# Kernel tuning notes

Hardware: AMD Instinct MI355X
Metric: run time of the kernel (lower is better)

## Reference

```python
import math
import jax, jax.numpy as jnp
import numpy as np

B, S, D, H = 4, 1024, 768, 12  # batch, seq, hidden, heads (ViT-Base)
HD = D // H                     # head size = 64
EPS = 1e-12                     # F.normalize eps


def setup_inputs() -> dict:
    key = jax.random.key(0)
    ks = jax.random.split(key, 7)
    s = 0.02
    return {
        "hidden_states": jax.random.normal(ks[0], (B, S, D), dtype=jnp.float32),
        "Wq": jax.random.normal(ks[1], (D, D), dtype=jnp.float32) * s,
        "bq": jax.random.normal(ks[2], (D,), dtype=jnp.float32) * s,
        "Wv": jax.random.normal(ks[3], (D, D), dtype=jnp.float32) * s,
        "bv": jax.random.normal(ks[4], (D,), dtype=jnp.float32) * s,
        "Wo": jax.random.normal(ks[5], (D, D), dtype=jnp.float32) * s,
        "bo": jax.random.normal(ks[6], (D,), dtype=jnp.float32) * s,
    }


def _split_heads(x):
    # [B,S,D] -> [B,H,S,hd]
    b, s, _ = x.shape
    return x.reshape(b, s, H, HD).transpose(0, 2, 1, 3)


def reference(hidden_states, Wq, bq, Wv, bv, Wo, bo):
    b, s, d_model = hidden_states.shape
    # Linear layers (torch Linear: x @ W^T + b; here W stored already transposed)
    mixed_q = hidden_states @ Wq + bq          # key == query in this module
    mixed_v = hidden_states @ Wv + bv
    q = _split_heads(mixed_q)                  # [B,H,S,hd]
    v = _split_heads(mixed_v)                  # [B,H,S,hd]

    # symmetric self-attention (Q @ Q^T)
    scores = jnp.einsum("bhsd,bhtd->bhst", q, q) / math.sqrt(HD)
    probs1 = jax.nn.softmax(scores, axis=-1)                 # [B,H,S,S]
    probs = 0.5 * (probs1 + probs1.transpose(0, 1, 3, 2))    # symmetrize

    # F.normalize(value_layer, dim=2): L2-normalize along the SEQUENCE axis
    vnorm = jnp.maximum(jnp.sqrt(jnp.sum(v * v, axis=2, keepdims=True)), EPS)
    V = v / vnorm                                            # [B,H,S,hd]

    # random-walk Laplacian: D^{-1}(D - P) = I - P / rowsum  (diag structure exploited,
    # same math as diag_embed + matmul in the original)
    dvec = probs.sum(axis=3)                                 # [B,H,S]
    Pn = probs / dvec[..., :, None]                          # D^{-1} P
    LrwV = V - jnp.einsum("bhst,bhtd->bhsd", Pn, V)          # L_rw @ V

    # trace( sum_{b,h} V^T L_rw V ) = sum over all (b,h,s,d) of V * (L_rw V)
    denom = jnp.float32(HD * H * b)
    tr = jnp.abs(jnp.sum(V * LrwV)) / denom

    # orthogonality regularizer: sum (V^T V - I)^2
    VtV = jnp.einsum("bhsd,bhse->bhde", V, V)                # [B,H,hd,hd]
    regular_term = jnp.sum((VtV - jnp.eye(HD, dtype=V.dtype)) ** 2) / denom

    # context = P @ V  (is_last=False)
    ctx = jnp.einsum("bhst,bhtd->bhsd", probs, v)
    ctx = ctx.transpose(0, 2, 1, 3).reshape(b, s, d_model)
    attention_output = ctx @ Wo + bo                         # dropout = identity (p=0)
    return (attention_output, tr, regular_term, mixed_q, mixed_q)
```

## Files before the change

### kernel.cpp

```cpp
#include <hip/hip_runtime.h>
#include <math.h>

constexpr float SCALE = 0.125f;

typedef __attribute__((ext_vector_type(8))) short bf8;
typedef __attribute__((ext_vector_type(8))) unsigned short u16x8;
typedef __attribute__((ext_vector_type(4))) float f32x4;

static __device__ __forceinline__ unsigned short f2bf(float f) {
    unsigned int u = __float_as_uint(f);
    u += 0x7fffu + ((u >> 16) & 1u);
    return (unsigned short)(u >> 16);
}
static __device__ __forceinline__ float bf2f(unsigned short h) {
    return __uint_as_float(((unsigned int)h) << 16);
}
static __device__ __forceinline__ bf8 ld8(const unsigned short* p) {
    return *reinterpret_cast<const bf8*>(p);
}
static __device__ __forceinline__ unsigned int cvtpk(float lo, float hi) {
    unsigned int r;
    asm("v_cvt_pk_bf16_f32 %0, %1, %2" : "=v"(r) : "v"(lo), "v"(hi));
    return r;
}

__global__ __launch_bounds__(256)
void k_prep(const float* __restrict__ Wq, const float* __restrict__ Wv,
            unsigned short* __restrict__ WTq, unsigned short* __restrict__ WTv)
{
    __shared__ unsigned short T[64 * 72];
    const int bid = blockIdx.x;
    const bool isQ = (bid < 144);
    const int lb = isQ ? bid : bid - 144;
    const float* __restrict__ W = isQ ? Wq : Wv;
    unsigned short* __restrict__ WT = isQ ? WTq : WTv;
    const int n0 = (lb % 12) * 64;
    const int k0 = (lb / 12) * 64;
    const int tid = threadIdx.x;
    const int r  = tid >> 2;
    const int c0 = (tid & 3) * 16;
    const float* src = &W[(size_t)(k0 + r) * 768 + n0 + c0];
    #pragma unroll
    for (int q = 0; q < 4; ++q) {
        const float4 v = *reinterpret_cast<const float4*>(src + q * 4);
        uint2 pk;
        pk.x = cvtpk(v.x, v.y);
        pk.y = cvtpk(v.z, v.w);
        *reinterpret_cast<uint2*>(&T[r * 72 + c0 + q * 4]) = pk;
    }
    __syncthreads();
    const int n  = tid >> 2;
    const int kc = (tid & 3) * 16;
    u16x8 o0, o1;
    #pragma unroll
    for (int i = 0; i < 8; ++i) o0[i] = T[(kc + i) * 72 + n];
    #pragma unroll
    for (int i = 0; i < 8; ++i) o1[i] = T[(kc + 8 + i) * 72 + n];
    unsigned short* dst = WT + (size_t)(n0 + n) * 768 + k0 + kc;
    *reinterpret_cast<u16x8*>(dst)     = o0;
    *reinterpret_cast<u16x8*>(dst + 8) = o1;
}

__global__ __launch_bounds__(256)
void k_wt(const float* __restrict__ W, unsigned short* __restrict__ WT)
{
    __shared__ unsigned short T[64 * 72];
    const int n0 = blockIdx.x * 64;
    const int k0 = blockIdx.y * 64;
    const int tid = threadIdx.x;
    const int r  = tid >> 2;
    const int c0 = (tid & 3) * 16;
    const float* src = &W[(size_t)(k0 + r) * 768 + n0 + c0];
    #pragma unroll
    for (int q = 0; q < 4; ++q) {
        const float4 v = *reinterpret_cast<const float4*>(src + q * 4);
        uint2 pk;
        pk.x = cvtpk(v.x, v.y);
        pk.y = cvtpk(v.z, v.w);
        *reinterpret_cast<uint2*>(&T[r * 72 + c0 + q * 4]) = pk;
    }
    __syncthreads();
    const int n  = tid >> 2;
    const int kc = (tid & 3) * 16;
    u16x8 o0, o1;
    #pragma unroll
    for (int i = 0; i < 8; ++i) o0[i] = T[(kc + i) * 72 + n];
    #pragma unroll
    for (int i = 0; i < 8; ++i) o1[i] = T[(kc + 8 + i) * 72 + n];
    unsigned short* dst = WT + (size_t)(n0 + n) * 768 + k0 + kc;
    *reinterpret_cast<u16x8*>(dst)     = o0;
    *reinterpret_cast<u16x8*>(dst + 8) = o1;
}

__global__ __launch_bounds__(256)
void k_gemm_qv(const float* __restrict__ X,
               const unsigned short* __restrict__ WTq,
               const unsigned short* __restrict__ WTv,
               const float* __restrict__ bq, const float* __restrict__ bv,
               float* __restrict__ mq1, float* __restrict__ mq2,
               unsigned short* __restrict__ qb, unsigned short* __restrict__ mvb)
{
    __shared__ unsigned short As[64 * 72];
    __shared__ unsigned short Bs[128 * 72];
    const int m0 = blockIdx.x * 64;
    const bool isQ = (blockIdx.y < 6);
    const int n0 = (isQ ? blockIdx.y : blockIdx.y - 6) * 128;
    const unsigned short* __restrict__ WT = isQ ? WTq : WTv;
    const float* __restrict__ bias = isQ ? bq : bv;
    const int tid = threadIdx.x;
    const int wave = tid >> 6, lane = tid & 63, lm = lane & 15, lg = lane >> 4;
    const int wn = wave;

    f32x4 acc[4][2];
    #pragma unroll
    for (int mi = 0; mi < 4; ++mi)
        #pragma unroll
        for (int ni = 0; ni < 2; ++ni) acc[mi][ni] = (f32x4){0.f, 0.f, 0.f, 0.f};

    for (int k0 = 0; k0 < 768; k0 += 64) {
        #pragma unroll
        for (int it = 0; it < 4; ++it) {
            const int idx = tid + it * 256;
            const int arow = idx >> 4;
            const int ac4  = (idx & 15) * 4;
            const float4 v = *reinterpret_cast<const float4*>(
                &X[(size_t)(m0 + arow) * 768 + k0 + ac4]);
            uint2 pk;
            pk.x = cvtpk(v.x, v.y);
            pk.y = cvtpk(v.z, v.w);
            *reinterpret_cast<uint2*>(&As[arow * 72 + ac4]) = pk;
            const int brow = idx >> 3;
            const int bc8  = (idx & 7) * 8;
            *reinterpret_cast<u16x8*>(&Bs[brow * 72 + bc8]) =
                *reinterpret_cast<const u16x8*>(&WT[(size_t)(n0 + brow) * 768 + k0 + bc8]);
        }
        __syncthreads();
        #pragma unroll
        for (int ks = 0; ks < 2; ++ks) {
            bf8 af[4], bfr[2];
            #pragma unroll
            for (int mi = 0; mi < 4; ++mi)
                af[mi] = *reinterpret_cast<const bf8*>(
                    &As[(mi * 16 + lm) * 72 + ks * 32 + lg * 8]);
            #pragma unroll
            for (int ni = 0; ni < 2; ++ni)
                bfr[ni] = *reinterpret_cast<const bf8*>(
                    &Bs[(wn * 32 + ni * 16 + lm) * 72 + ks * 32 + lg * 8]);
            #pragma unroll
            for (int mi = 0; mi < 4; ++mi)
                #pragma unroll
                for (int ni = 0; ni < 2; ++ni)
                    acc[mi][ni] = __builtin_amdgcn_mfma_f32_16x16x32_bf16(
                        af[mi], bfr[ni], acc[mi][ni], 0, 0, 0);
        }
        __syncthreads();
    }
    #pragma unroll
    for (int ni = 0; ni < 2; ++ni) {
        const int c = n0 + wn * 32 + ni * 16 + lm;
        const float bcol = bias[c];
        #pragma unroll
        for (int mi = 0; mi < 4; ++mi)
            #pragma unroll
            for (int j = 0; j < 4; ++j) {
                const int r = m0 + mi * 16 + lg * 4 + j;
                const float v = acc[mi][ni][j] + bcol;
                const size_t off = (size_t)r * 768 + c;
                if (isQ) {
                    mq1[off] = v;
                    mq2[off] = v;
                    qb[off]  = f2bf(v);
                } else {
                    mvb[off] = f2bf(v);
                }
            }
    }
}

__global__ __launch_bounds__(256)
void k_gemm_one(const unsigned short* __restrict__ Xb,
                const unsigned short* __restrict__ WT,
                const float* __restrict__ bias, float* __restrict__ out)
{
    __shared__ unsigned short As[64 * 72];
    __shared__ unsigned short Bs[64 * 72];
    const int m0 = blockIdx.x * 64;
    const int n0 = blockIdx.y * 64;
    const int tid = threadIdx.x;
    const int w = tid >> 6, lane = tid & 63, lm = lane & 15, lg = lane >> 4;

    f32x4 acc[4];
    #pragma unroll
    for (int ni = 0; ni < 4; ++ni) acc[ni] = (f32x4){0.f, 0.f, 0.f, 0.f};

    for (int k0 = 0; k0 < 768; k0 += 64) {
        #pragma unroll
        for (int it = 0; it < 2; ++it) {
            const int idx = tid + it * 256;
            const int row = idx >> 3;
            const int c8  = (idx & 7) * 8;
            *reinterpret_cast<u16x8*>(&As[row * 72 + c8]) =
                *reinterpret_cast<const u16x8*>(&Xb[(size_t)(m0 + row) * 768 + k0 + c8]);
            *reinterpret_cast<u16x8*>(&Bs[row * 72 + c8]) =
                *reinterpret_cast<const u16x8*>(&WT[(size_t)(n0 + row) * 768 + k0 + c8]);
        }
        __syncthreads();
        #pragma unroll
        for (int ks = 0; ks < 2; ++ks) {
            const bf8 af = *reinterpret_cast<const bf8*>(
                &As[(w * 16 + lm) * 72 + ks * 32 + lg * 8]);
            #pragma unroll
            for (int ni = 0; ni < 4; ++ni) {
                const bf8 bfr = *reinterpret_cast<const bf8*>(
                    &Bs[(ni * 16 + lm) * 72 + ks * 32 + lg * 8]);
                acc[ni] = __builtin_amdgcn_mfma_f32_16x16x32_bf16(af, bfr, acc[ni], 0, 0, 0);
            }
        }
        __syncthreads();
    }
    #pragma unroll
    for (int ni = 0; ni < 4; ++ni) {
        const int c = n0 + ni * 16 + lm;
        const float bcol = bias[c];
        #pragma unroll
        for (int j = 0; j < 4; ++j) {
            const int r = m0 + w * 16 + lg * 4 + j;
            out[(size_t)r * 768 + c] = acc[ni][j] + bcol;
        }
    }
}

__global__ __launch_bounds__(256)
void k_pass1T(const unsigned short* __restrict__ qb,
              const unsigned short* __restrict__ mvb,
              unsigned short* __restrict__ vT,
              float* __restrict__ a, float* __restrict__ nrmp)
{
    __shared__ __align__(16) unsigned short Kb[2][64 * 72];
    const int bid = blockIdx.x;
    const int st = (bid >> 3) & 15;
    const int bh = (bid & 7) + 8 * (bid >> 7);
    const int b = bh / 12, h = bh % 12;
    const int s0 = st * 64;
    const int tid = threadIdx.x;
    const int w = tid >> 6, lane = tid & 63, lm = lane & 15, lg = lane >> 4;
    const size_t qoff = (size_t)(b * 1024) * 768 + h * 64;

    {
        const int r  = tid >> 2;
        const int c0 = (tid & 3) * 16;
        const unsigned short* src = mvb + (size_t)(b * 1024 + s0 + r) * 768 + h * 64 + c0;
        const u16x8 x0 = *reinterpret_cast<const u16x8*>(src);
        const u16x8 x1 = *reinterpret_cast<const u16x8*>(src + 8);
        *reinterpret_cast<u16x8*>(&Kb[0][r * 72 + c0])     = x0;
        *reinterpret_cast<u16x8*>(&Kb[0][r * 72 + c0 + 8]) = x1;
        __syncthreads();
        const int dd  = tid >> 2;
        const int sc0 = (tid & 3) * 16;
        u16x8 o0, o1;
        float ps = 0.f;
        #pragma unroll
        for (int k = 0; k < 8; ++k) {
            o0[k] = Kb[0][(sc0 + k) * 72 + dd];
            const float v = bf2f(o0[k]);
            ps = fmaf(v, v, ps);
        }
        #pragma unroll
        for (int k = 0; k < 8; ++k) {
            o1[k] = Kb[0][(sc0 + 8 + k) * 72 + dd];
            const float v = bf2f(o1[k]);
            ps = fmaf(v, v, ps);
        }
        ps += __shfl_xor(ps, 1);
        ps += __shfl_xor(ps, 2);
        if ((tid & 3) == 0) nrmp[(size_t)(bh * 16 + st) * 64 + dd] = ps;
        unsigned short* dst = vT + (size_t)bh * 65536 + (size_t)dd * 1024 + s0 + sc0;
        *reinterpret_cast<u16x8*>(dst)     = o0;
        *reinterpret_cast<u16x8*>(dst + 8) = o1;
        __syncthreads();
    }

    const unsigned short* srow_p = qb + qoff + (size_t)(s0 + 16 * w + lm) * 768;
    const bf8 qs0 = ld8(srow_p + 8 * lg);
    const bf8 qs1 = ld8(srow_p + 32 + 8 * lg);
    const f32x4 z = {0.f, 0.f, 0.f, 0.f};
    float r = 0.f;
    const int sr = tid >> 2;
    const int sc = (tid & 3) << 4;

    u16x8 kr0 = *reinterpret_cast<const u16x8*>(qb + qoff + (size_t)sr * 768 + sc);
    u16x8 kr1 = *reinterpret_cast<const u16x8*>(qb + qoff + (size_t)sr * 768 + sc + 8);
    *reinterpret_cast<u16x8*>(&Kb[0][sr * 72 + sc])     = kr0;
    *reinterpret_cast<u16x8*>(&Kb[0][sr * 72 + sc + 8]) = kr1;
    __syncthreads();
    int cur = 0;

    for (int tt = 0; tt < 16; ++tt) {
        if (tt < 15) {
            const size_t rg = qoff + (size_t)((tt + 1) * 64 + sr) * 768 + sc;
            kr0 = *reinterpret_cast<const u16x8*>(qb + rg);
            kr1 = *reinterpret_cast<const u16x8*>(qb + rg + 8);
        }
        #pragma unroll
        for (int nf = 0; nf < 4; ++nf) {
            const bf8 ka0 = *reinterpret_cast<const bf8*>(
                &Kb[cur][(16 * nf + lm) * 72 + 8 * lg]);
            const bf8 ka1 = *reinterpret_cast<const bf8*>(
                &Kb[cur][(16 * nf + lm) * 72 + 32 + 8 * lg]);
            f32x4 ef = __builtin_amdgcn_mfma_f32_16x16x32_bf16(ka0, qs0, z, 0, 0, 0);
            ef = __builtin_amdgcn_mfma_f32_16x16x32_bf16(ka1, qs1, ef, 0, 0, 0);
            r += __expf(ef[0] * SCALE) + __expf(ef[1] * SCALE)
               + __expf(ef[2] * SCALE) + __expf(ef[3] * SCALE);
        }
        if (tt < 15) {
            *reinterpret_cast<u16x8*>(&Kb[cur ^ 1][sr * 72 + sc])     = kr0;
            *reinterpret_cast<u16x8*>(&Kb[cur ^ 1][sr * 72 + sc + 8]) = kr1;
        }
        __syncthreads();
        cur ^= 1;
    }
    r += __shfl_xor(r, 16);
    r += __shfl_xor(r, 32);
    if (lg == 0) a[(size_t)bh * 1024 + s0 + 16 * w + lm] = 1.f / r;
}

__global__ __launch_bounds__(256)
void k_normfin(const float* __restrict__ nrmp, float* __restrict__ inv_n,
               float* __restrict__ t1p)
{
    const int bh = blockIdx.x;
    const int tid = threadIdx.x;
    __shared__ float t1s[64];
    if (tid < 64) {
        float s = 0.f;
        for (int st = 0; st < 16; ++st)
            s += nrmp[(size_t)(bh * 16 + st) * 64 + tid];
        const float n = fmaxf(sqrtf(s), 1e-12f);
        const float iv = 1.f / n;
        inv_n[bh * 64 + tid] = iv;
        t1s[tid] = s * iv * iv;
    }
    __syncthreads();
    if (tid == 0) {
        float t = 0.f;
        for (int k = 0; k < 64; ++k) t += t1s[k];
        t1p[bh] = t;
    }
}

__global__ __launch_bounds__(256)
void k_pass2(const unsigned short* __restrict__ qb,
             const unsigned short* __restrict__ vT,
             const unsigned short* __restrict__ mvb,
             const float* __restrict__ a,
             const float* __restrict__ invn,
             unsigned short* __restrict__ ctxb,
             float* __restrict__ t2p)
{
    __shared__ __align__(16) unsigned short Kb[2][64 * 72];
    __shared__ __align__(16) unsigned short Vb[2][64 * 72];
    __shared__ __align__(16) unsigned short F_lds[4 * 16 * 72];
    __shared__ float red[256];
    const int bid = blockIdx.x;
    const int st = (bid >> 3) & 15;
    const int bh = (bid & 7) + 8 * (bid >> 7);
    const int b = bh / 12, h = bh % 12;
    const int s0 = st * 64;
    const int tid = threadIdx.x;
    const int w = tid >> 6, lane = tid & 63, lm = lane & 15, lg = lane >> 4;
    const size_t qoff = (size_t)(b * 1024) * 768 + h * 64;
    const unsigned short* srow_p = qb + qoff + (size_t)(s0 + 16 * w + lm) * 768;
    const bf8 qs0 = ld8(srow_p + 8 * lg);
    const bf8 qs1 = ld8(srow_p + 32 + 8 * lg);
    const unsigned short* vbase = vT + (size_t)bh * 65536;
    const float* abase = a + (size_t)bh * 1024;
    const float a_s = abase[s0 + 16 * w + lm];
    unsigned short* Frow = &F_lds[w * 1152 + lm * 72];
    float inv2[4];
    #pragma unroll
    for (int nf = 0; nf < 4; ++nf) {
        const float iv = invn[bh * 64 + lm + 16 * nf];
        inv2[nf] = iv * iv;
    }
    const f32x4 z = {0.f, 0.f, 0.f, 0.f};
    f32x4 acc[4];
    #pragma unroll
    for (int nf = 0; nf < 4; ++nf) acc[nf] = z;
    float sF = 0.f;
    const int sr = tid >> 2;
    const int sc = (tid & 3) << 4;

    u16x8 kr0 = *reinterpret_cast<const u16x8*>(qb + qoff + (size_t)sr * 768 + sc);
    u16x8 kr1 = *reinterpret_cast<const u16x8*>(qb + qoff + (size_t)sr * 768 + sc + 8);
    u16x8 vr0 = *reinterpret_cast<const u16x8*>(vbase + (size_t)sr * 1024 + sc);
    u16x8 vr1 = *reinterpret_cast<const u16x8*>(vbase + (size_t)sr * 1024 + sc + 8);
    *reinterpret_cast<u16x8*>(&Kb[0][sr * 72 + sc])     = kr0;
    *reinterpret_cast<u16x8*>(&Kb[0][sr * 72 + sc + 8]) = kr1;
    *reinterpret_cast<u16x8*>(&Vb[0][sr * 72 + sc])     = vr0;
    *reinterpret_cast<u16x8*>(&Vb[0][sr * 72 + sc + 8]) = vr1;
    __syncthreads();
    int cur = 0;

    for (int tt = 0; tt < 16; ++tt) {
        const int t0 = tt * 64;
        if (tt < 15) {
            const size_t kg = qoff + (size_t)(t0 + 64 + sr) * 768 + sc;
            kr0 = *reinterpret_cast<const u16x8*>(qb + kg);
            kr1 = *reinterpret_cast<const u16x8*>(qb + kg + 8);
            const size_t vg = (size_t)sr * 1024 + t0 + 64 + sc;
            vr0 = *reinterpret_cast<const u16x8*>(vbase + vg);
            vr1 = *reinterpret_cast<const u16x8*>(vbase + vg + 8);
        }
        f32x4 ef[4];
        #pragma unroll
        for (int nf = 0; nf < 4; ++nf) {
            const bf8 ka0 = *reinterpret_cast<const bf8*>(
                &Kb[cur][(16 * nf + lm) * 72 + 8 * lg]);
            const bf8 ka1 = *reinterpret_cast<const bf8*>(
                &Kb[cur][(16 * nf + lm) * 72 + 32 + 8 * lg]);
            ef[nf] = __builtin_amdgcn_mfma_f32_16x16x32_bf16(ka0, qs0, z, 0, 0, 0);
            ef[nf] = __builtin_amdgcn_mfma_f32_16x16x32_bf16(ka1, qs1, ef[nf], 0, 0, 0);
        }
        #pragma unroll
        for (int nf = 0; nf < 4; ++nf) {
            const float4 af = *reinterpret_cast<const float4*>(
                abase + t0 + 16 * nf + 4 * lg);
            const float f0 = __expf(ef[nf][0] * SCALE) * (a_s + af.x);
            const float f1 = __expf(ef[nf][1] * SCALE) * (a_s + af.y);
            const float f2 = __expf(ef[nf][2] * SCALE) * (a_s + af.z);
            const float f3 = __expf(ef[nf][3] * SCALE) * (a_s + af.w);
            sF += (f0 + f1) + (f2 + f3);
            uint2 pk;
            pk.x = cvtpk(f0, f1);
            pk.y = cvtpk(f2, f3);
            *reinterpret_cast<uint2*>(&Frow[16 * nf + 4 * lg]) = pk;
        }
        #pragma unroll
        for (int ks = 0; ks < 2; ++ks) {
            const bf8 fa = *reinterpret_cast<const bf8*>(&Frow[32 * ks + 8 * lg]);
            #pragma unroll
            for (int nf = 0; nf < 4; ++nf) {
                const bf8 vfr = *reinterpret_cast<const bf8*>(
                    &Vb[cur][(16 * nf + lm) * 72 + 32 * ks + 8 * lg]);
                acc[nf] = __builtin_amdgcn_mfma_f32_16x16x32_bf16(fa, vfr, acc[nf], 0, 0, 0);
            }
        }
        if (tt < 15) {
            *reinterpret_cast<u16x8*>(&Kb[cur ^ 1][sr * 72 + sc])     = kr0;
            *reinterpret_cast<u16x8*>(&Kb[cur ^ 1][sr * 72 + sc + 8]) = kr1;
            *reinterpret_cast<u16x8*>(&Vb[cur ^ 1][sr * 72 + sc])     = vr0;
            *reinterpret_cast<u16x8*>(&Vb[cur ^ 1][sr * 72 + sc + 8]) = vr1;
        }
        __syncthreads();
        cur ^= 1;
    }
    sF += __shfl_xor(sF, 16);
    sF += __shfl_xor(sF, 32);

    float t2 = 0.f;
    #pragma unroll
    for (int j = 0; j < 4; ++j) {
        const int srow = s0 + 16 * w + 4 * lg + j;
        const float sFj = __shfl(sF, 4 * lg + j);
        const float rdv = 2.f / sFj;
        const size_t rowoff = (size_t)(b * 1024 + srow) * 768 + h * 64;
        #pragma unroll
        for (int nf = 0; nf < 4; ++nf) {
            const int d = lm + 16 * nf;
            const float cf = 0.5f * acc[nf][j];
            ctxb[rowoff + d] = f2bf(cf);
            const float vv = bf2f(mvb[rowoff + d]);
            t2 = fmaf(vv * cf, inv2[nf] * rdv, t2);
        }
    }
    red[tid] = t2;
    __syncthreads();
    for (int k = 128; k >= 1; k >>= 1) {
        if (tid < k) red[tid] += red[tid + k];
        __syncthreads();
    }
    if (tid == 0) t2p[bh * 16 + st] = red[0];
}

__global__ __launch_bounds__(256)
void k_reg(const unsigned short* __restrict__ vT, const float* __restrict__ invn,
           float* __restrict__ regp)
{
    const int bh = blockIdx.x;
    const int tid = threadIdx.x;
    const int w = tid >> 6, lane = tid & 63, lm = lane & 15, lg = lane >> 4;
    const unsigned short* base = vT + (size_t)bh * 65536;
    const unsigned short* arowp = base + (size_t)(16 * w + lm) * 1024;
    const f32x4 z = {0.f, 0.f, 0.f, 0.f};
    f32x4 acc[4];
    #pragma unroll
    for (int nf = 0; nf < 4; ++nf) acc[nf] = z;
    for (int kb = 0; kb < 32; ++kb) {
        const int t0 = kb * 32 + 8 * lg;
        const bf8 av = ld8(arowp + t0);
        #pragma unroll
        for (int nf = 0; nf < 4; ++nf) {
            const bf8 bv = ld8(base + (size_t)(lm + 16 * nf) * 1024 + t0);
            acc[nf] = __builtin_amdgcn_mfma_f32_16x16x32_bf16(av, bv, acc[nf], 0, 0, 0);
        }
    }
    float part = 0.f;
    #pragma unroll
    for (int nf = 0; nf < 4; ++nf) {
        const int d2 = lm + 16 * nf;
        const float i2 = invn[bh * 64 + d2];
        #pragma unroll
        for (int j = 0; j < 4; ++j) {
            const int d1 = 16 * w + 4 * lg + j;
            const float g = acc[nf][j] * invn[bh * 64 + d1] * i2;
            const float diff = g - ((d1 == d2) ? 1.f : 0.f);
            part = fmaf(diff, diff, part);
        }
    }
    __shared__ float red[256];
    red[tid] = part;
    __syncthreads();
    for (int k = 128; k >= 1; k >>= 1) {
        if (tid < k) red[tid] += red[tid + k];
        __syncthreads();
    }
    if (tid == 0) regp[bh] = red[0];
}

__global__ __launch_bounds__(256)
void k_final(const float* __restrict__ t1p, const float* __restrict__ t2p,
             const float* __restrict__ regp, float* __restrict__ out_tr,
             float* __restrict__ out_reg)
{
    const int tid = threadIdx.x;
    float s1 = 0.f, s2 = 0.f, s3 = 0.f;
    for (int i = tid; i < 768; i += 256) s2 += t2p[i];
    if (tid < 48) { s1 = t1p[tid]; s3 = regp[tid]; }
    __shared__ float R1[256];
    __shared__ float R2[256];
    __shared__ float R3[256];
    R1[tid] = s1; R2[tid] = s2; R3[tid] = s3;
    __syncthreads();
    for (int w = 128; w >= 1; w >>= 1) {
        if (tid < w) { R1[tid] += R1[tid + w]; R2[tid] += R2[tid + w]; R3[tid] += R3[tid + w]; }
        __syncthreads();
    }
    if (tid == 0) {
        *out_tr  = fabsf(R1[0] - R2[0]) / 3072.f;
        *out_reg = R3[0] / 3072.f;
    }
}

extern "C" void kernel_launch(void* const* d_in, const int* in_sizes, int n_in,
                              void* d_out, int out_size, void* d_ws, size_t ws_size,
                              hipStream_t stream)
{
    const float* X  = (const float*)d_in[0];
    const float* Wq = (const float*)d_in[1];
    const float* bq = (const float*)d_in[2];
    const float* Wv = (const float*)d_in[3];
    const float* bv = (const float*)d_in[4];
    const float* Wo = (const float*)d_in[5];
    const float* bo = (const float*)d_in[6];

    float* out = (float*)d_out;
    float* att = out;
    float* tr  = out + 3145728;
    float* rg  = out + 3145729;
    float* mq1 = out + 3145730;
    float* mq2 = out + 6291458;

    float* ws = (float*)d_ws;
    unsigned short* mvb  = (unsigned short*)(ws);
    unsigned short* qb   = (unsigned short*)(ws + 1572864);
    unsigned short* vTslot = (unsigned short*)(ws + 3145728);
    unsigned short* WTq  = vTslot;
    unsigned short* WTv  = vTslot + 589824;
    unsigned short* vT   = vTslot;
    unsigned short* WTo  = vTslot;
    unsigned short* ctxb = (unsigned short*)(ws + 4718592);
    float* nrmp = ws + 6291456;
    float* aarr = ws + 6389760;
    float* invn = ws + 6438960;
    float* t1p  = ws + 6442032;
    float* t2p  = ws + 6442080;
    float* regp = ws + 6442848;

    if (ws_size < (size_t)6442896 * sizeof(float)) return;

    k_prep     <<<288,          256, 0, stream>>>(Wq, Wv, WTq, WTv);
    k_gemm_qv  <<<dim3(64, 12), 256, 0, stream>>>(X, WTq, WTv, bq, bv, mq1, mq2, qb, mvb);
    k_pass1T   <<<768,          256, 0, stream>>>(qb, mvb, vT, aarr, nrmp);
    k_normfin  <<<48,           256, 0, stream>>>(nrmp, invn, t1p);
    k_pass2    <<<768,          256, 0, stream>>>(qb, vT, mvb, aarr, invn, ctxb, t2p);
    k_reg      <<<48,           256, 0, stream>>>(vT, invn, regp);
    k_final    <<<1,            256, 0, stream>>>(t1p, t2p, regp, tr, rg);
    k_wt       <<<dim3(12, 12), 256, 0, stream>>>(Wo, WTo);
    k_gemm_one <<<dim3(64, 12), 256, 0, stream>>>(ctxb, WTo, bo, att);
}
```

Before: 126.0 us.

## Fuse norm finalize and Gram regularizer into pass2, add MFMA priority hints

Removes the k_normfin and k_reg kernels. Each pass2 block now recomputes the inverse norms from the partial sums into shared memory, and the st==0 blocks accumulate the V^T V Gram matrix from the V tiles already staged in LDS. The trace term t1 moves into k_final, and s_setprio hints are placed around the MFMA sections in pass1T and pass2. This saves two launches and a separate full read of vT, at the cost of extra MFMA work and imbalance in the st==0 blocks, plus redundant norm recomputation in every block.

```diff
diff --git a/kernel.cpp b/kernel.cpp
--- a/kernel.cpp
+++ b/kernel.cpp
@@ -301,6 +301,7 @@
             kr0 = *reinterpret_cast<const u16x8*>(qb + rg);
             kr1 = *reinterpret_cast<const u16x8*>(qb + rg + 8);
         }
+        __builtin_amdgcn_s_setprio(1);
         #pragma unroll
         for (int nf = 0; nf < 4; ++nf) {
             const bf8 ka0 = *reinterpret_cast<const bf8*>(
@@ -312,6 +313,7 @@
             r += __expf(ef[0] * SCALE) + __expf(ef[1] * SCALE)
                + __expf(ef[2] * SCALE) + __expf(ef[3] * SCALE);
         }
+        __builtin_amdgcn_s_setprio(0);
         if (tt < 15) {
             *reinterpret_cast<u16x8*>(&Kb[cur ^ 1][sr * 72 + sc])     = kr0;
             *reinterpret_cast<u16x8*>(&Kb[cur ^ 1][sr * 72 + sc + 8]) = kr1;
@@ -322,30 +324,6 @@
     r += __shfl_xor(r, 16);
     r += __shfl_xor(r, 32);
     if (lg == 0) a[(size_t)bh * 1024 + s0 + 16 * w + lm] = 1.f / r;
-}
-
-__global__ __launch_bounds__(256)
-void k_normfin(const float* __restrict__ nrmp, float* __restrict__ inv_n,
-               float* __restrict__ t1p)
-{
-    const int bh = blockIdx.x;
-    const int tid = threadIdx.x;
-    __shared__ float t1s[64];
-    if (tid < 64) {
-        float s = 0.f;
-        for (int st = 0; st < 16; ++st)
-            s += nrmp[(size_t)(bh * 16 + st) * 64 + tid];
-        const float n = fmaxf(sqrtf(s), 1e-12f);
-        const float iv = 1.f / n;
-        inv_n[bh * 64 + tid] = iv;
-        t1s[tid] = s * iv * iv;
-    }
-    __syncthreads();
-    if (tid == 0) {
-        float t = 0.f;
-        for (int k = 0; k < 64; ++k) t += t1s[k];
-        t1p[bh] = t;
-    }
 }
 
 __global__ __launch_bounds__(256)
@@ -353,14 +331,15 @@
              const unsigned short* __restrict__ vT,
              const unsigned short* __restrict__ mvb,
              const float* __restrict__ a,
-             const float* __restrict__ invn,
+             const float* __restrict__ nrmp,
              unsigned short* __restrict__ ctxb,
-             float* __restrict__ t2p)
+             float* __restrict__ t2p, float* __restrict__ regp)
 {
     __shared__ __align__(16) unsigned short Kb[2][64 * 72];
     __shared__ __align__(16) unsigned short Vb[2][64 * 72];
     __shared__ __align__(16) unsigned short F_lds[4 * 16 * 72];
     __shared__ float red[256];
+    __shared__ float inv_sh[64];
     const int bid = blockIdx.x;
     const int st = (bid >> 3) & 15;
     const int bh = (bid & 7) + 8 * (bid >> 7);
@@ -376,19 +355,21 @@
     const float* abase = a + (size_t)bh * 1024;
     const float a_s = abase[s0 + 16 * w + lm];
     unsigned short* Frow = &F_lds[w * 1152 + lm * 72];
-    float inv2[4];
-    #pragma unroll
-    for (int nf = 0; nf < 4; ++nf) {
-        const float iv = invn[bh * 64 + lm + 16 * nf];
-        inv2[nf] = iv * iv;
-    }
     const f32x4 z = {0.f, 0.f, 0.f, 0.f};
-    f32x4 acc[4];
-    #pragma unroll
-    for (int nf = 0; nf < 4; ++nf) acc[nf] = z;
+    f32x4 acc[4], gacc[4];
+    #pragma unroll
+    for (int nf = 0; nf < 4; ++nf) { acc[nf] = z; gacc[nf] = z; }
     float sF = 0.f;
     const int sr = tid >> 2;
     const int sc = (tid & 3) << 4;
+    const bool doGram = (st == 0);
+
+    if (tid < 64) {
+        float s = 0.f;
+        #pragma unroll
+        for (int t = 0; t < 16; ++t) s += nrmp[(size_t)(bh * 16 + t) * 64 + tid];
+        inv_sh[tid] = 1.f / fmaxf(sqrtf(s), 1e-12f);
+    }
 
     u16x8 kr0 = *reinterpret_cast<const u16x8*>(qb + qoff + (size_t)sr * 768 + sc);
     u16x8 kr1 = *reinterpret_cast<const u16x8*>(qb + qoff + (size_t)sr * 768 + sc + 8);
@@ -401,6 +382,13 @@
     __syncthreads();
     int cur = 0;
 
+    float inv2[4];
+    #pragma unroll
+    for (int nf = 0; nf < 4; ++nf) {
+        const float iv = inv_sh[lm + 16 * nf];
+        inv2[nf] = iv * iv;
+    }
+
     for (int tt = 0; tt < 16; ++tt) {
         const int t0 = tt * 64;
         if (tt < 15) {
@@ -412,6 +400,7 @@
             vr1 = *reinterpret_cast<const u16x8*>(vbase + vg + 8);
         }
         f32x4 ef[4];
+        __builtin_amdgcn_s_setprio(1);
         #pragma unroll
         for (int nf = 0; nf < 4; ++nf) {
             const bf8 ka0 = *reinterpret_cast<const bf8*>(
@@ -421,6 +410,7 @@
             ef[nf] = __builtin_amdgcn_mfma_f32_16x16x32_bf16(ka0, qs0, z, 0, 0, 0);
             ef[nf] = __builtin_amdgcn_mfma_f32_16x16x32_bf16(ka1, qs1, ef[nf], 0, 0, 0);
         }
+        __builtin_amdgcn_s_setprio(0);
         #pragma unroll
         for (int nf = 0; nf < 4; ++nf) {
             const float4 af = *reinterpret_cast<const float4*>(
@@ -435,16 +425,24 @@
             pk.y = cvtpk(f2, f3);
             *reinterpret_cast<uint2*>(&Frow[16 * nf + 4 * lg]) = pk;
         }
+        __builtin_amdgcn_s_setprio(1);
         #pragma unroll
         for (int ks = 0; ks < 2; ++ks) {
             const bf8 fa = *reinterpret_cast<const bf8*>(&Frow[32 * ks + 8 * lg]);
+            bf8 ga;
+            if (doGram)
+                ga = *reinterpret_cast<const bf8*>(
+                    &Vb[cur][(16 * w + lm) * 72 + 32 * ks + 8 * lg]);
             #pragma unroll
             for (int nf = 0; nf < 4; ++nf) {
                 const bf8 vfr = *reinterpret_cast<const bf8*>(
                     &Vb[cur][(16 * nf + lm) * 72 + 32 * ks + 8 * lg]);
                 acc[nf] = __builtin_amdgcn_mfma_f32_16x16x32_bf16(fa, vfr, acc[nf], 0, 0, 0);
+                if (doGram)
+                    gacc[nf] = __builtin_amdgcn_mfma_f32_16x16x32_bf16(ga, vfr, gacc[nf], 0, 0, 0);
             }
         }
+        __builtin_amdgcn_s_setprio(0);
         if (tt < 15) {
             *reinterpret_cast<u16x8*>(&Kb[cur ^ 1][sr * 72 + sc])     = kr0;
             *reinterpret_cast<u16x8*>(&Kb[cur ^ 1][sr * 72 + sc + 8]) = kr1;
@@ -480,62 +478,49 @@
         __syncthreads();
     }
     if (tid == 0) t2p[bh * 16 + st] = red[0];
-}
-
-__global__ __launch_bounds__(256)
-void k_reg(const unsigned short* __restrict__ vT, const float* __restrict__ invn,
-           float* __restrict__ regp)
-{
-    const int bh = blockIdx.x;
-    const int tid = threadIdx.x;
-    const int w = tid >> 6, lane = tid & 63, lm = lane & 15, lg = lane >> 4;
-    const unsigned short* base = vT + (size_t)bh * 65536;
-    const unsigned short* arowp = base + (size_t)(16 * w + lm) * 1024;
-    const f32x4 z = {0.f, 0.f, 0.f, 0.f};
-    f32x4 acc[4];
-    #pragma unroll
-    for (int nf = 0; nf < 4; ++nf) acc[nf] = z;
-    for (int kb = 0; kb < 32; ++kb) {
-        const int t0 = kb * 32 + 8 * lg;
-        const bf8 av = ld8(arowp + t0);
+
+    if (doGram) {
+        float part = 0.f;
         #pragma unroll
         for (int nf = 0; nf < 4; ++nf) {
-            const bf8 bv = ld8(base + (size_t)(lm + 16 * nf) * 1024 + t0);
-            acc[nf] = __builtin_amdgcn_mfma_f32_16x16x32_bf16(av, bv, acc[nf], 0, 0, 0);
-        }
-    }
-    float part = 0.f;
-    #pragma unroll
-    for (int nf = 0; nf < 4; ++nf) {
-        const int d2 = lm + 16 * nf;
-        const float i2 = invn[bh * 64 + d2];
-        #pragma unroll
-        for (int j = 0; j < 4; ++j) {
-            const int d1 = 16 * w + 4 * lg + j;
-            const float g = acc[nf][j] * invn[bh * 64 + d1] * i2;
-            const float diff = g - ((d1 == d2) ? 1.f : 0.f);
-            part = fmaf(diff, diff, part);
-        }
-    }
-    __shared__ float red[256];
-    red[tid] = part;
-    __syncthreads();
-    for (int k = 128; k >= 1; k >>= 1) {
-        if (tid < k) red[tid] += red[tid + k];
-        __syncthreads();
-    }
-    if (tid == 0) regp[bh] = red[0];
-}
-
-__global__ __launch_bounds__(256)
-void k_final(const float* __restrict__ t1p, const float* __restrict__ t2p,
+            const int d2 = 16 * nf + lm;
+            const float i2 = inv_sh[d2];
+            #pragma unroll
+            for (int j = 0; j < 4; ++j) {
+                const int d1 = 16 * w + 4 * lg + j;
+                const float g = gacc[nf][j] * inv_sh[d1] * i2;
+                const float diff = g - ((d1 == d2) ? 1.f : 0.f);
+                part = fmaf(diff, diff, part);
+            }
+        }
+        __syncthreads();
+        red[tid] = part;
+        __syncthreads();
+        for (int k = 128; k >= 1; k >>= 1) {
+            if (tid < k) red[tid] += red[tid + k];
+            __syncthreads();
+        }
+        if (tid == 0) regp[bh] = red[0];
+    }
+}
+
+__global__ __launch_bounds__(256)
+void k_final(const float* __restrict__ nrmp, const float* __restrict__ t2p,
              const float* __restrict__ regp, float* __restrict__ out_tr,
              float* __restrict__ out_reg)
 {
     const int tid = threadIdx.x;
     float s1 = 0.f, s2 = 0.f, s3 = 0.f;
+    for (int i = tid; i < 3072; i += 256) {
+        const int bh = i >> 6, d = i & 63;
+        float s = 0.f;
+        #pragma unroll
+        for (int t = 0; t < 16; ++t) s += nrmp[(size_t)(bh * 16 + t) * 64 + d];
+        const float iv = 1.f / fmaxf(sqrtf(s), 1e-12f);
+        s1 = fmaf(s, iv * iv, s1);
+    }
     for (int i = tid; i < 768; i += 256) s2 += t2p[i];
-    if (tid < 48) { s1 = t1p[tid]; s3 = regp[tid]; }
+    if (tid < 48) s3 = regp[tid];
     __shared__ float R1[256];
     __shared__ float R2[256];
     __shared__ float R3[256];
@@ -581,8 +566,6 @@
     unsigned short* ctxb = (unsigned short*)(ws + 4718592);
     float* nrmp = ws + 6291456;
     float* aarr = ws + 6389760;
-    float* invn = ws + 6438960;
-    float* t1p  = ws + 6442032;
     float* t2p  = ws + 6442080;
     float* regp = ws + 6442848;
 
@@ -591,10 +574,8 @@
     k_prep     <<<288,          256, 0, stream>>>(Wq, Wv, WTq, WTv);
     k_gemm_qv  <<<dim3(64, 12), 256, 0, stream>>>(X, WTq, WTv, bq, bv, mq1, mq2, qb, mvb);
     k_pass1T   <<<768,          256, 0, stream>>>(qb, mvb, vT, aarr, nrmp);
-    k_normfin  <<<48,           256, 0, stream>>>(nrmp, invn, t1p);
-    k_pass2    <<<768,          256, 0, stream>>>(qb, vT, mvb, aarr, invn, ctxb, t2p);
-    k_reg      <<<48,           256, 0, stream>>>(vT, invn, regp);
-    k_final    <<<1,            256, 0, stream>>>(t1p, t2p, regp, tr, rg);
+    k_pass2    <<<768,          256, 0, stream>>>(qb, vT, mvb, aarr, nrmp, ctxb, t2p, regp);
     k_wt       <<<dim3(12, 12), 256, 0, stream>>>(Wo, WTo);
     k_gemm_one <<<dim3(64, 12), 256, 0, stream>>>(ctxb, WTo, bo, att);
-}
+    k_final    <<<1,            256, 0, stream>>>(nrmp, t2p, regp, tr, rg);
+}
```

Result: slower. 133.7 us (+6.1%).

## Split the Gram-matrix regularizer over the sequence and reduce partials separately

Applied to the files above, without the earlier changes.

The V^T V regularizer kernel previously ran only 48 blocks, each looping over the full 1024-long sequence. It now runs a 48x8 grid where each block covers one eighth of the sequence and writes its raw 64x64 partial Gram matrix into workspace that reuses the dead qb region. A new k_regfin kernel sums the eight partials, applies the inverse norms and reduces the squared deviation from the identity. The point is to fill more compute units; the cost is an extra launch plus a write and read-back of the partial matrices. The weight-transpose kernel is also moved earlier so it runs between the two regularizer kernels.

```diff
diff --git a/kernel.cpp b/kernel.cpp
--- a/kernel.cpp
+++ b/kernel.cpp
@@ -483,10 +483,10 @@
 }
 
 __global__ __launch_bounds__(256)
-void k_reg(const unsigned short* __restrict__ vT, const float* __restrict__ invn,
-           float* __restrict__ regp)
+void k_reg(const unsigned short* __restrict__ vT, float* __restrict__ Gpart)
 {
     const int bh = blockIdx.x;
+    const int q  = blockIdx.y;
     const int tid = threadIdx.x;
     const int w = tid >> 6, lane = tid & 63, lm = lane & 15, lg = lane >> 4;
     const unsigned short* base = vT + (size_t)bh * 65536;
@@ -495,8 +495,9 @@
     f32x4 acc[4];
     #pragma unroll
     for (int nf = 0; nf < 4; ++nf) acc[nf] = z;
-    for (int kb = 0; kb < 32; ++kb) {
-        const int t0 = kb * 32 + 8 * lg;
+    #pragma unroll
+    for (int kk = 0; kk < 4; ++kk) {
+        const int t0 = (q * 4 + kk) * 32 + 8 * lg;
         const bf8 av = ld8(arowp + t0);
         #pragma unroll
         for (int nf = 0; nf < 4; ++nf) {
@@ -504,18 +505,34 @@
             acc[nf] = __builtin_amdgcn_mfma_f32_16x16x32_bf16(av, bv, acc[nf], 0, 0, 0);
         }
     }
-    float part = 0.f;
+    float* gdst = Gpart + (size_t)(bh * 8 + q) * 4096;
     #pragma unroll
     for (int nf = 0; nf < 4; ++nf) {
         const int d2 = lm + 16 * nf;
-        const float i2 = invn[bh * 64 + d2];
         #pragma unroll
         for (int j = 0; j < 4; ++j) {
             const int d1 = 16 * w + 4 * lg + j;
-            const float g = acc[nf][j] * invn[bh * 64 + d1] * i2;
-            const float diff = g - ((d1 == d2) ? 1.f : 0.f);
-            part = fmaf(diff, diff, part);
-        }
+            gdst[d1 * 64 + d2] = acc[nf][j];
+        }
+    }
+}
+
+__global__ __launch_bounds__(256)
+void k_regfin(const float* __restrict__ Gpart, const float* __restrict__ invn,
+              float* __restrict__ regp)
+{
+    const int bh = blockIdx.x;
+    const int tid = threadIdx.x;
+    float part = 0.f;
+    for (int c = tid; c < 4096; c += 256) {
+        const int d1 = c >> 6, d2 = c & 63;
+        float g = 0.f;
+        #pragma unroll
+        for (int q = 0; q < 8; ++q)
+            g += Gpart[(size_t)(bh * 8 + q) * 4096 + c];
+        g *= invn[bh * 64 + d1] * invn[bh * 64 + d2];
+        const float diff = g - ((d1 == d2) ? 1.f : 0.f);
+        part = fmaf(diff, diff, part);
     }
     __shared__ float red[256];
     red[tid] = part;
@@ -573,6 +590,7 @@
     float* ws = (float*)d_ws;
     unsigned short* mvb  = (unsigned short*)(ws);
     unsigned short* qb   = (unsigned short*)(ws + 1572864);
+    float*          Gpart = ws + 1572864;
     unsigned short* vTslot = (unsigned short*)(ws + 3145728);
     unsigned short* WTq  = vTslot;
     unsigned short* WTv  = vTslot + 589824;
@@ -593,8 +611,9 @@
     k_pass1T   <<<768,          256, 0, stream>>>(qb, mvb, vT, aarr, nrmp);
     k_normfin  <<<48,           256, 0, stream>>>(nrmp, invn, t1p);
     k_pass2    <<<768,          256, 0, stream>>>(qb, vT, mvb, aarr, invn, ctxb, t2p);
-    k_reg      <<<48,           256, 0, stream>>>(vT, invn, regp);
+    k_reg      <<<dim3(48, 8),  256, 0, stream>>>(vT, Gpart);
+    k_wt       <<<dim3(12, 12), 256, 0, stream>>>(Wo, WTo);
+    k_regfin   <<<48,           256, 0, stream>>>(Gpart, invn, regp);
+    k_gemm_one <<<dim3(64, 12), 256, 0, stream>>>(ctxb, WTo, bo, att);
     k_final    <<<1,            256, 0, stream>>>(t1p, t2p, regp, tr, rg);
-    k_wt       <<<dim3(12, 12), 256, 0, stream>>>(Wo, WTo);
-    k_gemm_one <<<dim3(64, 12), 256, 0, stream>>>(ctxb, WTo, bo, att);
-}
+}
```

After: 124.1 us. No clear change (-1.5%).
